# Performance work log

Measured on AMD Instinct MI355X. Metric: run time of the kernel, lower is better.

The kernel has to match this reference:

```python
import jax, jax.numpy as jnp
import numpy as np

B, T, HID = 1, 4096, 1024
H, HKV, D = 16, 4, 64          # query heads, kv heads, head_dim
G = H // HKV                    # gqa groups; repeat '(h g)' -> q head idx = h*G + g
EPS = 1e-6
SCALE = 1.0 / np.sqrt(D)


def setup_inputs() -> dict:
    key = jax.random.key(0)
    ks = jax.random.split(key, 8)
    hidden_states = jax.random.normal(ks[0], (B, T, HID), dtype=jnp.float32)
    # real rotary tables, shape [1, T, D//2]
    inv_freq = 1.0 / (10000.0 ** (jnp.arange(0, D // 2, dtype=jnp.float32) / (D // 2)))
    theta = jnp.arange(T, dtype=jnp.float32)[:, None] * inv_freq[None, :]
    cos = jnp.cos(theta)[None]
    sin = jnp.sin(theta)[None]
    s = 1.0 / np.sqrt(HID)
    Wq = jax.random.normal(ks[1], (HID, H * D), dtype=jnp.float32) * s
    Wk = jax.random.normal(ks[2], (HID, HKV * D), dtype=jnp.float32) * s
    Wv = jax.random.normal(ks[3], (HID, HKV * D), dtype=jnp.float32) * s
    Wo = jax.random.normal(ks[4], (H * D, HID), dtype=jnp.float32) * s
    q_norm_w = jnp.ones((D,), dtype=jnp.float32)
    k_norm_w = jnp.ones((D,), dtype=jnp.float32)
    return dict(hidden_states=hidden_states, cos=cos, sin=sin, Wq=Wq, Wk=Wk,
                Wv=Wv, Wo=Wo, q_norm_w=q_norm_w, k_norm_w=k_norm_w)


def _rmsnorm(x, w):
    xf = x.astype(jnp.float32)
    n = xf * jax.lax.rsqrt(jnp.mean(xf * xf, axis=-1, keepdims=True) + EPS)
    return (n * w).astype(x.dtype)


def _rope(x, cos, sin):
    # x: [b, t, h, d]; cos/sin: [1, t, d//2] -> [1, t, 1, d//2]
    half = x.shape[-1] // 2
    x1, x2 = x[..., :half], x[..., half:]
    c = cos[:, :x.shape[1], None, :]
    s = sin[:, :x.shape[1], None, :]
    return jnp.concatenate([x1 * c - x2 * s, x1 * s + x2 * c], axis=-1)


def reference(hidden_states, cos, sin, Wq, Wk, Wv, Wo, q_norm_w, k_norm_w):
    b, t, _ = hidden_states.shape
    q = (hidden_states @ Wq).reshape(b, t, H, D)
    k = (hidden_states @ Wk).reshape(b, t, HKV, D)
    v = (hidden_states @ Wv).reshape(b, t, HKV, D)
    q = _rmsnorm(q, q_norm_w)
    k = _rmsnorm(k, k_norm_w)
    q = _rope(q, cos, sin)
    k = _rope(k, cos, sin)
    # GQA without materializing repeated K/V: q head idx = kv_head*G + group
    qg = q.reshape(b, t, HKV, G, D)
    scores = jnp.einsum('bqhgd,bkhd->bhgqk', qg, k) * SCALE
    causal = jnp.tril(jnp.ones((t, t), dtype=bool))  # flex block_mask = causal decoder mask
    scores = jnp.where(causal, scores, jnp.finfo(scores.dtype).min)
    p = jax.nn.softmax(scores, axis=-1)
    out = jnp.einsum('bhgqk,bkhd->bqhgd', p, v).reshape(b, t, H * D)
    return out @ Wo
```

## Files before the change

### kernel.cpp

```cpp
#include <hip/hip_runtime.h>
#include <stdint.h>

#define TT 4096
#define HIDD 1024

typedef __attribute__((ext_vector_type(4))) float f32x4;
typedef __attribute__((ext_vector_type(8))) short s16x8;

static constexpr float kEps = 1e-6f;
static constexpr float kCsc = 0.125f * 1.44269504088896f;

static constexpr size_t OFF_HS   = 0;
static constexpr size_t OFF_WQKV = 8388608;
static constexpr size_t OFF_WO   = 11534336;
static constexpr size_t OFF_QKV  = 13631488;
static constexpr size_t OFF_Q    = 0;
static constexpr size_t OFF_K    = 8388608;
static constexpr size_t OFF_VT   = 38797312;
static constexpr size_t OFF_O    = 13631488;

__device__ __forceinline__ unsigned int pk_bf16(float a, float b) {
  union { float f; unsigned int u; } x, y;
  x.f = a; y.f = b;
  unsigned int lo = (x.u + 0x7fffu + ((x.u >> 16) & 1u)) >> 16;
  unsigned int hi = (y.u + 0x7fffu + ((y.u >> 16) & 1u)) >> 16;
  return (lo & 0xffffu) | (hi << 16);
}
__device__ __forceinline__ unsigned short bf16_1(float a) {
  union { float f; unsigned int u; } x; x.f = a;
  return (unsigned short)((x.u + 0x7fffu + ((x.u >> 16) & 1u)) >> 16);
}
__device__ __forceinline__ unsigned int cvtpk(float lo, float hi) {
  unsigned int r;
  asm("v_cvt_pk_bf16_f32 %0, %1, %2" : "=v"(r) : "v"(lo), "v"(hi));
  return r;
}
__device__ __forceinline__ void gload16(const void* g, void* l) {
  __builtin_amdgcn_global_load_lds(
      (const __attribute__((address_space(1))) unsigned int*)g,
      (__attribute__((address_space(3))) unsigned int*)l, 16, 0, 0);
}

__global__ void k_convert_hs(const float* __restrict__ hs, unsigned short* __restrict__ out) {
  int idx = blockIdx.x * 256 + threadIdx.x;
  int t = idx >> 7, kc = idx & 127;
  const float4* src = (const float4*)(hs + (size_t)t * HIDD + kc * 8);
  float4 a = src[0], b = src[1];
  int kcs = (kc & ~7) | ((kc & 7) ^ (t & 7));
  uint4 w;
  w.x = pk_bf16(a.x, a.y); w.y = pk_bf16(a.z, a.w);
  w.z = pk_bf16(b.x, b.y); w.w = pk_bf16(b.z, b.w);
  *(uint4*)(out + (size_t)t * HIDD + kcs * 8) = w;
}

__global__ void k_convert_w_all(const float* __restrict__ Wq, const float* __restrict__ Wk,
                                const float* __restrict__ Wv, const float* __restrict__ Wo,
                                unsigned short* __restrict__ wqkv, unsigned short* __restrict__ wo_t) {
  int b = blockIdx.x, tid = threadIdx.x;
  const float* W; unsigned short* outT; int nshift, idx;
  if (b < 512)      { W = Wq; outT = wqkv;                nshift = 10; idx = b * 256 + tid; }
  else if (b < 640) { W = Wk; outT = wqkv + 1024 * 1024;  nshift = 8;  idx = (b - 512) * 256 + tid; }
  else if (b < 768) { W = Wv; outT = wqkv + 1280 * 1024;  nshift = 8;  idx = (b - 640) * 256 + tid; }
  else              { W = Wo; outT = wo_t;                nshift = 10; idx = (b - 768) * 256 + tid; }
  int ncols = 1 << nshift;
  int kc = idx >> nshift, n = idx & (ncols - 1);
  float v[8];
#pragma unroll
  for (int e = 0; e < 8; ++e) v[e] = W[(size_t)(kc * 8 + e) * ncols + n];
  int kcs = (kc & ~7) | ((kc & 7) ^ (n & 7));
  uint4 w;
  w.x = pk_bf16(v[0], v[1]); w.y = pk_bf16(v[2], v[3]);
  w.z = pk_bf16(v[4], v[5]); w.w = pk_bf16(v[6], v[7]);
  *(uint4*)(outT + (size_t)n * HIDD + kcs * 8) = w;
}

__global__ __launch_bounds__(512) void k_gemm(const unsigned short* __restrict__ A,
                                              const unsigned short* __restrict__ Bt,
                                              float* __restrict__ C, int M, int N, int K) {
  __shared__ __attribute__((aligned(16))) unsigned short As[2][128 * 64];
  __shared__ __attribute__((aligned(16))) unsigned short Bs[2][128 * 64];
  const int tid = threadIdx.x;
  const int m0 = blockIdx.y * 128, n0 = blockIdx.x * 128;
  const int wid = tid >> 6, lane = tid & 63;
  const int g = lane >> 4, qi = lane & 15;
  const int wr = wid >> 2, wc = wid & 3;
  const int srow = tid >> 3, schk = tid & 7;
  f32x4 acc[4][2] = {};
  const int nkt = K >> 6;

  auto STAGE = [&](int b, int k0) {
#pragma unroll
    for (int j = 0; j < 2; ++j) {
      int ra = j * 64 + srow;
      gload16(A + (size_t)(m0 + ra) * K + k0 + schk * 8,
              (char*)&As[b][0] + j * 8192 + (wid << 10));
      gload16(Bt + (size_t)(n0 + ra) * K + k0 + schk * 8,
              (char*)&Bs[b][0] + j * 8192 + (wid << 10));
    }
  };

  STAGE(0, 0);
  __syncthreads();
  int cur = 0;
  for (int kt = 0; kt < nkt; ++kt) {
    if (kt + 1 < nkt) STAGE(cur ^ 1, (kt + 1) << 6);
#pragma unroll
    for (int kh = 0; kh < 2; ++kh) {
      s16x8 af[4], bq[2];
#pragma unroll
      for (int i = 0; i < 4; ++i) {
        int rA = wr * 64 + i * 16 + qi;
        af[i] = *(const s16x8*)((const char*)&As[cur][0] + rA * 128 + ((((kh << 2) | g) ^ (rA & 7)) << 4));
      }
#pragma unroll
      for (int jn = 0; jn < 2; ++jn) {
        int rB = wc * 32 + jn * 16 + qi;
        bq[jn] = *(const s16x8*)((const char*)&Bs[cur][0] + rB * 128 + ((((kh << 2) | g) ^ (rB & 7)) << 4));
      }
      __builtin_amdgcn_s_setprio(1);
#pragma unroll
      for (int i = 0; i < 4; ++i)
#pragma unroll
        for (int jn = 0; jn < 2; ++jn)
          acc[i][jn] = __builtin_amdgcn_mfma_f32_16x16x32_bf16(af[i], bq[jn], acc[i][jn], 0, 0, 0);
      __builtin_amdgcn_s_setprio(0);
    }
    __syncthreads();
    cur ^= 1;
  }
#pragma unroll
  for (int i = 0; i < 4; ++i)
#pragma unroll
    for (int jn = 0; jn < 2; ++jn) {
      int row = m0 + wr * 64 + i * 16 + g * 4;
      int col = n0 + wc * 32 + jn * 16 + qi;
#pragma unroll
      for (int r = 0; r < 4; ++r)
        C[(size_t)(row + r) * N + col] = acc[i][jn][r];
    }
}

__global__ void k_prep(const float* __restrict__ qkv, const float* __restrict__ cosb,
                       const float* __restrict__ sinb, const float* __restrict__ qw,
                       const float* __restrict__ kw, unsigned short* __restrict__ qo,
                       unsigned short* __restrict__ ko) {
  int rowid = blockIdx.x * 4 + (threadIdx.x >> 6);
  int lane = threadIdx.x & 63;
  int t = rowid / 20, slot = rowid % 20;
  float x = qkv[(size_t)t * 1536 + slot * 64 + lane];
  float ss = x * x;
#pragma unroll
  for (int off = 32; off; off >>= 1) ss += __shfl_xor(ss, off);
  float n = x * rsqrtf(ss * (1.0f / 64.0f) + kEps);
  n *= (slot < 16) ? qw[lane] : kw[lane];
  float c = cosb[t * 32 + (lane & 31)];
  float s = sinb[t * 32 + (lane & 31)];
  float other = __shfl_xor(n, 32);
  float r = (lane < 32) ? (n * c - other * s) : (other * s + n * c);
  if (slot < 16) {
    unsigned short b = bf16_1(r * kCsc);
    qo[((size_t)slot * TT + t) * 64 + lane] = b;
  } else {
    unsigned short b = bf16_1(r);
    int hv = slot - 16;
    int d = (((lane >> 3) ^ (t & 7)) << 3) | (lane & 7);
    ko[((size_t)hv * TT + t) * 64 + d] = b;
  }
}

__global__ void k_vT(const float* __restrict__ qkv, unsigned short* __restrict__ vt) {
  __shared__ float tile[64][65];
  int t0 = blockIdx.x * 64, hv = blockIdx.y, tid = threadIdx.x;
  int cc = tid & 63, rr0 = tid >> 6;
#pragma unroll
  for (int i = 0; i < 16; ++i) {
    int r = rr0 * 16 + i;
    tile[r][cc] = qkv[(size_t)(t0 + r) * 1536 + 1280 + hv * 64 + cc];
  }
  __syncthreads();
#pragma unroll
  for (int jj = 0; jj < 2; ++jj) {
    int idx = jj * 256 + tid;
    int d = idx >> 3, tc = idx & 7;
    uint4 w;
    w.x = pk_bf16(tile[tc * 8 + 0][d], tile[tc * 8 + 1][d]);
    w.y = pk_bf16(tile[tc * 8 + 2][d], tile[tc * 8 + 3][d]);
    w.z = pk_bf16(tile[tc * 8 + 4][d], tile[tc * 8 + 5][d]);
    w.w = pk_bf16(tile[tc * 8 + 6][d], tile[tc * 8 + 7][d]);
    int tcs = tc ^ (d & 7);
    *(uint4*)(vt + ((size_t)hv * 64 + d) * TT + t0 + tcs * 8) = w;
  }
}

__global__ __launch_bounds__(512) void k_attn(const unsigned short* __restrict__ q,
                                              const unsigned short* __restrict__ kk,
                                              const unsigned short* __restrict__ vt,
                                              unsigned short* __restrict__ o) {
  __shared__ __attribute__((aligned(16))) unsigned short Kl[2][64 * 64];
  __shared__ __attribute__((aligned(16))) unsigned short Vl[2][64 * 64];
  __shared__ __attribute__((aligned(16))) unsigned short Pl[8][1536];
  const int tid = threadIdx.x;
  const int bid = blockIdx.x;
  const int work = (bid & 7) * 64 + (bid >> 3);
  const int h = work >> 5;
  const int i0 = work & 31;
  const int hv = h >> 2;
  const int wid = tid >> 6, lane = tid & 63, g = lane >> 4, qi = lane & 15;
  const int qt = (wid < 4) ? i0 : (63 - i0);
  const int smax = 63 - i0;
  char* pb = (char*)&Pl[wid][0];

  auto STAGE = [&](int b, int s) {
    const int kv0 = s * 64;
    const int r = wid * 8 + (lane >> 3), c8 = (lane & 7) * 8;
    gload16(kk + ((size_t)hv * TT + kv0 + r) * 64 + c8, (char*)&Kl[b][0] + (wid << 10));
    gload16(vt + ((size_t)hv * 64 + r) * TT + kv0 + c8, (char*)&Vl[b][0] + (wid << 10));
  };

  const int qg = qt * 64 + (wid & 3) * 16 + qi;
  s16x8 qf[2];
#pragma unroll
  for (int kh = 0; kh < 2; ++kh)
    qf[kh] = *(const s16x8*)(q + ((size_t)h * TT + qg) * 64 + kh * 32 + g * 8);
  f32x4 acc[4] = {};
  float l0 = 0.0f, l1 = 0.0f;

  STAGE(0, 0);
  __syncthreads();
  int cur = 0;
  for (int s = 0; s <= smax; ++s) {
    if (s < smax) STAGE(cur ^ 1, s + 1);
    if (s <= qt) {
      const int kv0 = s * 64;
      f32x4 sacc[4] = {};
#pragma unroll
      for (int kh = 0; kh < 2; ++kh) {
        s16x8 kf[4];
#pragma unroll
        for (int cf = 0; cf < 4; ++cf) {
          int row = cf * 16 + qi;
          kf[cf] = *(const s16x8*)((const char*)&Kl[cur][0] + row * 128 + ((((kh << 2) | g) ^ (row & 7)) << 4));
        }
        __builtin_amdgcn_s_setprio(1);
#pragma unroll
        for (int cf = 0; cf < 4; ++cf)
          sacc[cf] = __builtin_amdgcn_mfma_f32_16x16x32_bf16(kf[cf], qf[kh], sacc[cf], 0, 0, 0);
        __builtin_amdgcn_s_setprio(0);
      }
      float pv[16];
      if (s == qt) {
#pragma unroll
        for (int cf = 0; cf < 4; ++cf)
#pragma unroll
          for (int r = 0; r < 4; ++r) {
            float v = sacc[cf][r];
            if ((kv0 + cf * 16 + g * 4 + r) > qg) v = -1e30f;
            pv[cf * 4 + r] = v;
          }
      } else {
#pragma unroll
        for (int cf = 0; cf < 4; ++cf)
#pragma unroll
          for (int r = 0; r < 4; ++r) pv[cf * 4 + r] = sacc[cf][r];
      }
#pragma unroll
      for (int i = 0; i < 8; ++i) {
        float e0 = exp2f(pv[2 * i]), e1 = exp2f(pv[2 * i + 1]);
        pv[2 * i] = e0; pv[2 * i + 1] = e1;
        l0 += e0; l1 += e1;
      }
#pragma unroll
      for (int cf = 0; cf < 4; ++cf) {
        int chunk = cf * 2 + (g >> 1);
        int base = qi * 128 + ((chunk ^ (qi & 7)) << 4) + ((g & 1) << 3);
        uint2 pw;
        pw.x = cvtpk(pv[cf * 4 + 0], pv[cf * 4 + 1]);
        pw.y = cvtpk(pv[cf * 4 + 2], pv[cf * 4 + 3]);
        *(uint2*)(pb + base) = pw;
      }
#pragma unroll
      for (int kh = 0; kh < 2; ++kh) {
        s16x8 pf = *(const s16x8*)(pb + qi * 128 + ((((kh << 2) | g) ^ (qi & 7)) << 4));
        s16x8 vf[4];
#pragma unroll
        for (int cf = 0; cf < 4; ++cf) {
          int row = cf * 16 + qi;
          vf[cf] = *(const s16x8*)((const char*)&Vl[cur][0] + row * 128 + ((((kh << 2) | g) ^ (row & 7)) << 4));
        }
        __builtin_amdgcn_s_setprio(1);
#pragma unroll
        for (int cf = 0; cf < 4; ++cf)
          acc[cf] = __builtin_amdgcn_mfma_f32_16x16x32_bf16(vf[cf], pf, acc[cf], 0, 0, 0);
        __builtin_amdgcn_s_setprio(0);
      }
    }
    __syncthreads();
    cur ^= 1;
  }
  float l_run = l0 + l1;
  l_run += __shfl_xor(l_run, 16);
  l_run += __shfl_xor(l_run, 32);
  float inv = 1.0f / l_run;
#pragma unroll
  for (int cf = 0; cf < 4; ++cf) {
    int col = h * 64 + cf * 16 + g * 4;
    int chunk = col >> 3;
    int chs = (chunk & ~7) | ((chunk & 7) ^ (qg & 7));
    char* ob = (char*)o + (size_t)qg * 2048 + (chs << 4) + ((g & 1) << 3);
    *(unsigned int*)ob = cvtpk(acc[cf][0] * inv, acc[cf][1] * inv);
    *(unsigned int*)(ob + 4) = cvtpk(acc[cf][2] * inv, acc[cf][3] * inv);
  }
}

extern "C" void kernel_launch(void* const* d_in, const int* in_sizes, int n_in,
                              void* d_out, int out_size, void* d_ws, size_t ws_size,
                              hipStream_t stream) {
  const float* hs   = (const float*)d_in[0];
  const float* cosb = (const float*)d_in[1];
  const float* sinb = (const float*)d_in[2];
  const float* Wq   = (const float*)d_in[3];
  const float* Wk   = (const float*)d_in[4];
  const float* Wv   = (const float*)d_in[5];
  const float* Wo   = (const float*)d_in[6];
  const float* qw   = (const float*)d_in[7];
  const float* kw   = (const float*)d_in[8];
  char* ws = (char*)d_ws;
  unsigned short* hs_swz = (unsigned short*)(ws + OFF_HS);
  unsigned short* wqkv   = (unsigned short*)(ws + OFF_WQKV);
  unsigned short* wo_t   = (unsigned short*)(ws + OFF_WO);
  float*          qkv    = (float*)(ws + OFF_QKV);
  unsigned short* qbf    = (unsigned short*)(ws + OFF_Q);
  unsigned short* kbf    = (unsigned short*)(ws + OFF_K);
  unsigned short* vtb    = (unsigned short*)(ws + OFF_VT);
  unsigned short* obf    = (unsigned short*)(ws + OFF_O);

  k_convert_hs<<<2048, 256, 0, stream>>>(hs, hs_swz);
  k_convert_w_all<<<1280, 256, 0, stream>>>(Wq, Wk, Wv, Wo, wqkv, wo_t);
  k_gemm<<<dim3(12, 32), 512, 0, stream>>>(hs_swz, wqkv, qkv, 4096, 1536, 1024);
  k_prep<<<20480, 256, 0, stream>>>(qkv, cosb, sinb, qw, kw, qbf, kbf);
  k_vT<<<dim3(64, 4), 256, 0, stream>>>(qkv, vtb);
  k_attn<<<512, 512, 0, stream>>>(qbf, kbf, vtb, obf);
  k_gemm<<<dim3(8, 32), 512, 0, stream>>>(obf, wo_t, (float*)d_out, 4096, 1024, 1024);
}
```

Baseline: 143.6 us.

## Restructure attention to per-wave 16-row tiles reading K/V directly from global

Attention no longer stages K and V tiles through double-buffered LDS with block-wide barriers. Each wave now owns 16-query-row tiles, taking one long and one short tile to balance the causal work, and reads K and V fragments directly from global or L2. V is stored in a tile-blocked transposed layout and K without the swizzle, so that these direct loads are contiguous. The loop is software-pipelined so that the softmax and P·V step of the previous block overlaps with the QK of the current one, and exp2 uses raw v_exp_f32. The goal is to remove the LDS staging and __syncthreads cost, at the price of more global traffic and register pressure, with launch bounds set for two blocks per CU.

```diff
diff --git a/kernel.cpp b/kernel.cpp
--- a/kernel.cpp
+++ b/kernel.cpp
@@ -33,6 +33,11 @@
 __device__ __forceinline__ unsigned int cvtpk(float lo, float hi) {
   unsigned int r;
   asm("v_cvt_pk_bf16_f32 %0, %1, %2" : "=v"(r) : "v"(lo), "v"(hi));
+  return r;
+}
+__device__ __forceinline__ float fexp2(float x) {
+  float r;
+  asm("v_exp_f32 %0, %1\n\ts_nop 0" : "=v"(r) : "v"(x));
   return r;
 }
 __device__ __forceinline__ void gload16(const void* g, void* l) {
@@ -163,14 +168,14 @@
   } else {
     unsigned short b = bf16_1(r);
     int hv = slot - 16;
-    int d = (((lane >> 3) ^ (t & 7)) << 3) | (lane & 7);
-    ko[((size_t)hv * TT + t) * 64 + d] = b;
+    ko[((size_t)hv * TT + t) * 64 + lane] = b;
   }
 }
 
 __global__ void k_vT(const float* __restrict__ qkv, unsigned short* __restrict__ vt) {
   __shared__ float tile[64][65];
   int t0 = blockIdx.x * 64, hv = blockIdx.y, tid = threadIdx.x;
+  int blk = blockIdx.x;
   int cc = tid & 63, rr0 = tid >> 6;
 #pragma unroll
   for (int i = 0; i < 16; ++i) {
@@ -187,86 +192,50 @@
     w.y = pk_bf16(tile[tc * 8 + 2][d], tile[tc * 8 + 3][d]);
     w.z = pk_bf16(tile[tc * 8 + 4][d], tile[tc * 8 + 5][d]);
     w.w = pk_bf16(tile[tc * 8 + 6][d], tile[tc * 8 + 7][d]);
-    int tcs = tc ^ (d & 7);
-    *(uint4*)(vt + ((size_t)hv * 64 + d) * TT + t0 + tcs * 8) = w;
-  }
-}
-
-__global__ __launch_bounds__(512) void k_attn(const unsigned short* __restrict__ q,
-                                              const unsigned short* __restrict__ kk,
-                                              const unsigned short* __restrict__ vt,
-                                              unsigned short* __restrict__ o) {
-  __shared__ __attribute__((aligned(16))) unsigned short Kl[2][64 * 64];
-  __shared__ __attribute__((aligned(16))) unsigned short Vl[2][64 * 64];
-  __shared__ __attribute__((aligned(16))) unsigned short Pl[8][1536];
+    *(uint4*)(vt + (((size_t)hv * 64 + blk) * 64 + d) * 64 + tc * 8) = w;
+  }
+}
+
+__global__ __launch_bounds__(512, 2) void k_attn(const unsigned short* __restrict__ q,
+                                                 const unsigned short* __restrict__ kk,
+                                                 const unsigned short* __restrict__ vt,
+                                                 unsigned short* __restrict__ o) {
+  __shared__ __attribute__((aligned(16))) unsigned short Pl[8][1024];
   const int tid = threadIdx.x;
+  const int wid = tid >> 6, lane = tid & 63, g = lane >> 4, qi = lane & 15;
   const int bid = blockIdx.x;
-  const int work = (bid & 7) * 64 + (bid >> 3);
-  const int h = work >> 5;
-  const int i0 = work & 31;
-  const int hv = h >> 2;
-  const int wid = tid >> 6, lane = tid & 63, g = lane >> 4, qi = lane & 15;
-  const int qt = (wid < 4) ? i0 : (63 - i0);
-  const int smax = 63 - i0;
+  const int xcd = bid & 7, blk = bid >> 3;
+  const int p = blk * 8 + wid;
+  const int head = xcd * 2 + (p >> 7);
+  const int aa = p & 127;
+  const int hv = head >> 2;
   char* pb = (char*)&Pl[wid][0];
-
-  auto STAGE = [&](int b, int s) {
-    const int kv0 = s * 64;
-    const int r = wid * 8 + (lane >> 3), c8 = (lane & 7) * 8;
-    gload16(kk + ((size_t)hv * TT + kv0 + r) * 64 + c8, (char*)&Kl[b][0] + (wid << 10));
-    gload16(vt + ((size_t)hv * 64 + r) * TT + kv0 + c8, (char*)&Vl[b][0] + (wid << 10));
-  };
-
-  const int qg = qt * 64 + (wid & 3) * 16 + qi;
-  s16x8 qf[2];
-#pragma unroll
-  for (int kh = 0; kh < 2; ++kh)
-    qf[kh] = *(const s16x8*)(q + ((size_t)h * TT + qg) * 64 + kh * 32 + g * 8);
-  f32x4 acc[4] = {};
-  float l0 = 0.0f, l1 = 0.0f;
-
-  STAGE(0, 0);
-  __syncthreads();
-  int cur = 0;
-  for (int s = 0; s <= smax; ++s) {
-    if (s < smax) STAGE(cur ^ 1, s + 1);
-    if (s <= qt) {
-      const int kv0 = s * 64;
-      f32x4 sacc[4] = {};
-#pragma unroll
-      for (int kh = 0; kh < 2; ++kh) {
-        s16x8 kf[4];
-#pragma unroll
-        for (int cf = 0; cf < 4; ++cf) {
-          int row = cf * 16 + qi;
-          kf[cf] = *(const s16x8*)((const char*)&Kl[cur][0] + row * 128 + ((((kh << 2) | g) ^ (row & 7)) << 4));
-        }
-        __builtin_amdgcn_s_setprio(1);
-#pragma unroll
-        for (int cf = 0; cf < 4; ++cf)
-          sacc[cf] = __builtin_amdgcn_mfma_f32_16x16x32_bf16(kf[cf], qf[kh], sacc[cf], 0, 0, 0);
-        __builtin_amdgcn_s_setprio(0);
-      }
-      float pv[16];
-      if (s == qt) {
-#pragma unroll
-        for (int cf = 0; cf < 4; ++cf)
-#pragma unroll
-          for (int r = 0; r < 4; ++r) {
-            float v = sacc[cf][r];
-            if ((kv0 + cf * 16 + g * 4 + r) > qg) v = -1e30f;
-            pv[cf * 4 + r] = v;
-          }
-      } else {
-#pragma unroll
-        for (int cf = 0; cf < 4; ++cf)
-#pragma unroll
-          for (int r = 0; r < 4; ++r) pv[cf * 4 + r] = sacc[cf][r];
-      }
-#pragma unroll
-      for (int i = 0; i < 8; ++i) {
-        float e0 = exp2f(pv[2 * i]), e1 = exp2f(pv[2 * i + 1]);
-        pv[2 * i] = e0; pv[2 * i + 1] = e1;
+  const unsigned short* kb = kk + ((size_t)hv * TT) * 64;
+
+  for (int half = 0; half < 2; ++half) {
+    const int t16 = half ? aa : (255 - aa);
+    const int nst = (t16 >> 2) + 1;
+    const int qg = t16 * 16 + qi;
+    s16x8 qf[2];
+#pragma unroll
+    for (int kh = 0; kh < 2; ++kh)
+      qf[kh] = *(const s16x8*)(q + ((size_t)head * TT + qg) * 64 + kh * 32 + g * 8);
+    f32x4 acc[4] = {};
+    float l0 = 0.0f, l1 = 0.0f;
+    float pv[16];
+
+    auto SMPV = [&](int s) {
+      const unsigned short* vb = vt + (((size_t)hv * 64 + s) * 64) * 64;
+      s16x8 vf[2][4];
+#pragma unroll
+      for (int kh = 0; kh < 2; ++kh)
+#pragma unroll
+        for (int cf = 0; cf < 4; ++cf)
+          vf[kh][cf] = *(const s16x8*)(vb + (size_t)(cf * 16 + qi) * 64 + kh * 32 + g * 8);
+#pragma unroll
+      for (int j = 0; j < 8; ++j) {
+        float e0 = fexp2(pv[2 * j]), e1 = fexp2(pv[2 * j + 1]);
+        pv[2 * j] = e0; pv[2 * j + 1] = e1;
         l0 += e0; l1 += e1;
       }
 #pragma unroll
@@ -281,34 +250,62 @@
 #pragma unroll
       for (int kh = 0; kh < 2; ++kh) {
         s16x8 pf = *(const s16x8*)(pb + qi * 128 + ((((kh << 2) | g) ^ (qi & 7)) << 4));
-        s16x8 vf[4];
-#pragma unroll
-        for (int cf = 0; cf < 4; ++cf) {
-          int row = cf * 16 + qi;
-          vf[cf] = *(const s16x8*)((const char*)&Vl[cur][0] + row * 128 + ((((kh << 2) | g) ^ (row & 7)) << 4));
-        }
         __builtin_amdgcn_s_setprio(1);
 #pragma unroll
         for (int cf = 0; cf < 4; ++cf)
-          acc[cf] = __builtin_amdgcn_mfma_f32_16x16x32_bf16(vf[cf], pf, acc[cf], 0, 0, 0);
+          acc[cf] = __builtin_amdgcn_mfma_f32_16x16x32_bf16(vf[kh][cf], pf, acc[cf], 0, 0, 0);
         __builtin_amdgcn_s_setprio(0);
       }
-    }
-    __syncthreads();
-    cur ^= 1;
-  }
-  float l_run = l0 + l1;
-  l_run += __shfl_xor(l_run, 16);
-  l_run += __shfl_xor(l_run, 32);
-  float inv = 1.0f / l_run;
-#pragma unroll
-  for (int cf = 0; cf < 4; ++cf) {
-    int col = h * 64 + cf * 16 + g * 4;
-    int chunk = col >> 3;
-    int chs = (chunk & ~7) | ((chunk & 7) ^ (qg & 7));
-    char* ob = (char*)o + (size_t)qg * 2048 + (chs << 4) + ((g & 1) << 3);
-    *(unsigned int*)ob = cvtpk(acc[cf][0] * inv, acc[cf][1] * inv);
-    *(unsigned int*)(ob + 4) = cvtpk(acc[cf][2] * inv, acc[cf][3] * inv);
+    };
+
+    for (int i = 0; i < nst; ++i) {
+      const int kv0 = i * 64;
+      s16x8 kf[2][4];
+#pragma unroll
+      for (int kh = 0; kh < 2; ++kh)
+#pragma unroll
+        for (int cf = 0; cf < 4; ++cf)
+          kf[kh][cf] = *(const s16x8*)(kb + (size_t)(kv0 + cf * 16 + qi) * 64 + kh * 32 + g * 8);
+      if (i > 0) SMPV(i - 1);
+      f32x4 sacc[4] = {};
+#pragma unroll
+      for (int kh = 0; kh < 2; ++kh) {
+        __builtin_amdgcn_s_setprio(1);
+#pragma unroll
+        for (int cf = 0; cf < 4; ++cf)
+          sacc[cf] = __builtin_amdgcn_mfma_f32_16x16x32_bf16(kf[kh][cf], qf[kh], sacc[cf], 0, 0, 0);
+        __builtin_amdgcn_s_setprio(0);
+      }
+      if (i == nst - 1) {
+#pragma unroll
+        for (int cf = 0; cf < 4; ++cf)
+#pragma unroll
+          for (int r = 0; r < 4; ++r) {
+            float v = sacc[cf][r];
+            pv[cf * 4 + r] = ((kv0 + cf * 16 + g * 4 + r) > qg) ? -1e30f : v;
+          }
+      } else {
+#pragma unroll
+        for (int cf = 0; cf < 4; ++cf)
+#pragma unroll
+          for (int r = 0; r < 4; ++r) pv[cf * 4 + r] = sacc[cf][r];
+      }
+    }
+    SMPV(nst - 1);
+
+    float l_run = l0 + l1;
+    l_run += __shfl_xor(l_run, 16);
+    l_run += __shfl_xor(l_run, 32);
+    float inv = 1.0f / l_run;
+#pragma unroll
+    for (int cf = 0; cf < 4; ++cf) {
+      int col = head * 64 + cf * 16 + g * 4;
+      int chunk = col >> 3;
+      int chs = (chunk & ~7) | ((chunk & 7) ^ (qg & 7));
+      char* ob = (char*)o + (size_t)qg * 2048 + (chs << 4) + ((g & 1) << 3);
+      *(unsigned int*)ob = cvtpk(acc[cf][0] * inv, acc[cf][1] * inv);
+      *(unsigned int*)(ob + 4) = cvtpk(acc[cf][2] * inv, acc[cf][3] * inv);
+    }
   }
 }
 
@@ -339,6 +336,6 @@
   k_gemm<<<dim3(12, 32), 512, 0, stream>>>(hs_swz, wqkv, qkv, 4096, 1536, 1024);
   k_prep<<<20480, 256, 0, stream>>>(qkv, cosb, sinb, qw, kw, qbf, kbf);
   k_vT<<<dim3(64, 4), 256, 0, stream>>>(qkv, vtb);
-  k_attn<<<512, 512, 0, stream>>>(qbf, kbf, vtb, obf);
+  k_attn<<<256, 512, 0, stream>>>(qbf, kbf, vtb, obf);
   k_gemm<<<dim3(8, 32), 512, 0, stream>>>(obf, wo_t, (float*)d_out, 4096, 1024, 1024);
 }
```

Result: slower. 302.5 us (+110.7%).

## Software-pipeline attention loop: overlap previous tile's softmax/PV with current QK

Applied to the files above, without the earlier changes.

Restructures the causal attention inner loop so the exp/softmax, P store and PV MFMAs for tile s-1 run after the K fragment loads for tile s and before its QK MFMAs. V fragments are preloaded into registers at the end of each step so they survive the double-buffer swap, and a trailing SMPV call drains the pipeline. The aim is to hide LDS load latency and exp work behind independent MFMA streams. In exchange it raises VGPR pressure (K and V fragments held together), which could reduce occupancy or cause spills.

```diff
diff --git a/kernel.cpp b/kernel.cpp
--- a/kernel.cpp
+++ b/kernel.cpp
@@ -224,79 +224,91 @@
     qf[kh] = *(const s16x8*)(q + ((size_t)h * TT + qg) * 64 + kh * 32 + g * 8);
   f32x4 acc[4] = {};
   float l0 = 0.0f, l1 = 0.0f;
+  float pv[16];
+  s16x8 vf[2][4];
+
+  auto SMPV = [&]() {
+#pragma unroll
+    for (int j = 0; j < 8; ++j) {
+      float e0 = exp2f(pv[2 * j]), e1 = exp2f(pv[2 * j + 1]);
+      pv[2 * j] = e0; pv[2 * j + 1] = e1;
+      l0 += e0; l1 += e1;
+    }
+#pragma unroll
+    for (int cf = 0; cf < 4; ++cf) {
+      int chunk = cf * 2 + (g >> 1);
+      int base = qi * 128 + ((chunk ^ (qi & 7)) << 4) + ((g & 1) << 3);
+      uint2 pw;
+      pw.x = cvtpk(pv[cf * 4 + 0], pv[cf * 4 + 1]);
+      pw.y = cvtpk(pv[cf * 4 + 2], pv[cf * 4 + 3]);
+      *(uint2*)(pb + base) = pw;
+    }
+#pragma unroll
+    for (int kh = 0; kh < 2; ++kh) {
+      s16x8 pf = *(const s16x8*)(pb + qi * 128 + ((((kh << 2) | g) ^ (qi & 7)) << 4));
+      __builtin_amdgcn_s_setprio(1);
+#pragma unroll
+      for (int cf = 0; cf < 4; ++cf)
+        acc[cf] = __builtin_amdgcn_mfma_f32_16x16x32_bf16(vf[kh][cf], pf, acc[cf], 0, 0, 0);
+      __builtin_amdgcn_s_setprio(0);
+    }
+  };
 
   STAGE(0, 0);
   __syncthreads();
   int cur = 0;
   for (int s = 0; s <= smax; ++s) {
     if (s < smax) STAGE(cur ^ 1, s + 1);
-    if (s <= qt) {
+    s16x8 kf[2][4];
+    const bool active = (s <= qt);
+    if (active) {
+#pragma unroll
+      for (int kh = 0; kh < 2; ++kh)
+#pragma unroll
+        for (int cf = 0; cf < 4; ++cf) {
+          int row = cf * 16 + qi;
+          kf[kh][cf] = *(const s16x8*)((const char*)&Kl[cur][0] + row * 128 + ((((kh << 2) | g) ^ (row & 7)) << 4));
+        }
+    }
+    if (s >= 1 && s <= qt + 1) SMPV();
+    if (active) {
       const int kv0 = s * 64;
       f32x4 sacc[4] = {};
 #pragma unroll
       for (int kh = 0; kh < 2; ++kh) {
-        s16x8 kf[4];
+        __builtin_amdgcn_s_setprio(1);
+#pragma unroll
+        for (int cf = 0; cf < 4; ++cf)
+          sacc[cf] = __builtin_amdgcn_mfma_f32_16x16x32_bf16(kf[kh][cf], qf[kh], sacc[cf], 0, 0, 0);
+        __builtin_amdgcn_s_setprio(0);
+      }
+      if (s == qt) {
+#pragma unroll
+        for (int cf = 0; cf < 4; ++cf)
+#pragma unroll
+          for (int r = 0; r < 4; ++r) {
+            float v = sacc[cf][r];
+            pv[cf * 4 + r] = ((kv0 + cf * 16 + g * 4 + r) > qg) ? -1e30f : v;
+          }
+      } else {
+#pragma unroll
+        for (int cf = 0; cf < 4; ++cf)
+#pragma unroll
+          for (int r = 0; r < 4; ++r) pv[cf * 4 + r] = sacc[cf][r];
+      }
+#pragma unroll
+      for (int kh = 0; kh < 2; ++kh)
 #pragma unroll
         for (int cf = 0; cf < 4; ++cf) {
           int row = cf * 16 + qi;
-          kf[cf] = *(const s16x8*)((const char*)&Kl[cur][0] + row * 128 + ((((kh << 2) | g) ^ (row & 7)) << 4));
+          vf[kh][cf] = *(const s16x8*)((const char*)&Vl[cur][0] + row * 128 + ((((kh << 2) | g) ^ (row & 7)) << 4));
         }
-        __builtin_amdgcn_s_setprio(1);
-#pragma unroll
-        for (int cf = 0; cf < 4; ++cf)
-          sacc[cf] = __builtin_amdgcn_mfma_f32_16x16x32_bf16(kf[cf], qf[kh], sacc[cf], 0, 0, 0);
-        __builtin_amdgcn_s_setprio(0);
-      }
-      float pv[16];
-      if (s == qt) {
-#pragma unroll
-        for (int cf = 0; cf < 4; ++cf)
-#pragma unroll
-          for (int r = 0; r < 4; ++r) {
-            float v = sacc[cf][r];
-            if ((kv0 + cf * 16 + g * 4 + r) > qg) v = -1e30f;
-            pv[cf * 4 + r] = v;
-          }
-      } else {
-#pragma unroll
-        for (int cf = 0; cf < 4; ++cf)
-#pragma unroll
-          for (int r = 0; r < 4; ++r) pv[cf * 4 + r] = sacc[cf][r];
-      }
-#pragma unroll
-      for (int i = 0; i < 8; ++i) {
-        float e0 = exp2f(pv[2 * i]), e1 = exp2f(pv[2 * i + 1]);
-        pv[2 * i] = e0; pv[2 * i + 1] = e1;
-        l0 += e0; l1 += e1;
-      }
-#pragma unroll
-      for (int cf = 0; cf < 4; ++cf) {
-        int chunk = cf * 2 + (g >> 1);
-        int base = qi * 128 + ((chunk ^ (qi & 7)) << 4) + ((g & 1) << 3);
-        uint2 pw;
-        pw.x = cvtpk(pv[cf * 4 + 0], pv[cf * 4 + 1]);
-        pw.y = cvtpk(pv[cf * 4 + 2], pv[cf * 4 + 3]);
-        *(uint2*)(pb + base) = pw;
-      }
-#pragma unroll
-      for (int kh = 0; kh < 2; ++kh) {
-        s16x8 pf = *(const s16x8*)(pb + qi * 128 + ((((kh << 2) | g) ^ (qi & 7)) << 4));
-        s16x8 vf[4];
-#pragma unroll
-        for (int cf = 0; cf < 4; ++cf) {
-          int row = cf * 16 + qi;
-          vf[cf] = *(const s16x8*)((const char*)&Vl[cur][0] + row * 128 + ((((kh << 2) | g) ^ (row & 7)) << 4));
-        }
-        __builtin_amdgcn_s_setprio(1);
-#pragma unroll
-        for (int cf = 0; cf < 4; ++cf)
-          acc[cf] = __builtin_amdgcn_mfma_f32_16x16x32_bf16(vf[cf], pf, acc[cf], 0, 0, 0);
-        __builtin_amdgcn_s_setprio(0);
-      }
     }
     __syncthreads();
     cur ^= 1;
   }
+  if (qt == smax) SMPV();
+
   float l_run = l0 + l1;
   l_run += __shfl_xor(l_run, 16);
   l_run += __shfl_xor(l_run, 32);
```

Measured after the change: 183.7 us. 1.28x slower.

## Split attention into smaller per-tile blocks and shrink GEMM tiles for occupancy

Applied to the files above, without the earlier changes.

The attention kernel changes from 512-thread blocks that paired complementary causal query tiles to 128-thread blocks. Each block handles one 64-row query tile, with every warp owning 32 query rows and reusing each K/V fragment across two MFMA row groups. Blocks are ordered longest-first and grouped by XCD to balance load. The GEMM moves to 256-thread blocks with 128x64 tiles, doubling the grid to raise occupancy and wave count, at the cost of less B-tile reuse per block.

```diff
diff --git a/kernel.cpp b/kernel.cpp
--- a/kernel.cpp
+++ b/kernel.cpp
@@ -74,28 +74,32 @@
   *(uint4*)(outT + (size_t)n * HIDD + kcs * 8) = w;
 }
 
-__global__ __launch_bounds__(512) void k_gemm(const unsigned short* __restrict__ A,
+__global__ __launch_bounds__(256) void k_gemm(const unsigned short* __restrict__ A,
                                               const unsigned short* __restrict__ Bt,
                                               float* __restrict__ C, int M, int N, int K) {
   __shared__ __attribute__((aligned(16))) unsigned short As[2][128 * 64];
-  __shared__ __attribute__((aligned(16))) unsigned short Bs[2][128 * 64];
+  __shared__ __attribute__((aligned(16))) unsigned short Bs[2][64 * 64];
   const int tid = threadIdx.x;
-  const int m0 = blockIdx.y * 128, n0 = blockIdx.x * 128;
+  const int m0 = blockIdx.y * 128, n0 = blockIdx.x * 64;
   const int wid = tid >> 6, lane = tid & 63;
   const int g = lane >> 4, qi = lane & 15;
-  const int wr = wid >> 2, wc = wid & 3;
-  const int srow = tid >> 3, schk = tid & 7;
+  const int wr = wid >> 1, wc = wid & 1;
+  const int srow = lane >> 3, schk = lane & 7;
   f32x4 acc[4][2] = {};
   const int nkt = K >> 6;
 
   auto STAGE = [&](int b, int k0) {
 #pragma unroll
+    for (int j = 0; j < 4; ++j) {
+      int ra = j * 32 + wid * 8 + srow;
+      gload16(A + (size_t)(m0 + ra) * K + k0 + schk * 8,
+              (char*)&As[b][0] + j * 4096 + (wid << 10));
+    }
+#pragma unroll
     for (int j = 0; j < 2; ++j) {
-      int ra = j * 64 + srow;
-      gload16(A + (size_t)(m0 + ra) * K + k0 + schk * 8,
-              (char*)&As[b][0] + j * 8192 + (wid << 10));
-      gload16(Bt + (size_t)(n0 + ra) * K + k0 + schk * 8,
-              (char*)&Bs[b][0] + j * 8192 + (wid << 10));
+      int rb = j * 32 + wid * 8 + srow;
+      gload16(Bt + (size_t)(n0 + rb) * K + k0 + schk * 8,
+              (char*)&Bs[b][0] + j * 4096 + (wid << 10));
     }
   };
 
@@ -192,123 +196,145 @@
   }
 }
 
-__global__ __launch_bounds__(512) void k_attn(const unsigned short* __restrict__ q,
-                                              const unsigned short* __restrict__ kk,
-                                              const unsigned short* __restrict__ vt,
-                                              unsigned short* __restrict__ o) {
+__global__ __launch_bounds__(128, 2) void k_attn(const unsigned short* __restrict__ q,
+                                                 const unsigned short* __restrict__ kk,
+                                                 const unsigned short* __restrict__ vt,
+                                                 unsigned short* __restrict__ o) {
   __shared__ __attribute__((aligned(16))) unsigned short Kl[2][64 * 64];
   __shared__ __attribute__((aligned(16))) unsigned short Vl[2][64 * 64];
-  __shared__ __attribute__((aligned(16))) unsigned short Pl[8][1536];
+  __shared__ __attribute__((aligned(16))) unsigned short Pl[2][2048];
   const int tid = threadIdx.x;
+  const int wid = tid >> 6, lane = tid & 63, g = lane >> 4, qi = lane & 15;
   const int bid = blockIdx.x;
-  const int work = (bid & 7) * 64 + (bid >> 3);
-  const int h = work >> 5;
-  const int i0 = work & 31;
-  const int hv = h >> 2;
-  const int wid = tid >> 6, lane = tid & 63, g = lane >> 4, qi = lane & 15;
-  const int qt = (wid < 4) ? i0 : (63 - i0);
-  const int smax = 63 - i0;
+  const int xcd = bid & 7, j = bid >> 3;
+  const int head = xcd * 2 + (j & 1);
+  const int qt = 63 - (j >> 1);
+  const int hv = head >> 2;
   char* pb = (char*)&Pl[wid][0];
+  const int srow = lane >> 3, schk8 = (lane & 7) * 8;
 
   auto STAGE = [&](int b, int s) {
     const int kv0 = s * 64;
-    const int r = wid * 8 + (lane >> 3), c8 = (lane & 7) * 8;
-    gload16(kk + ((size_t)hv * TT + kv0 + r) * 64 + c8, (char*)&Kl[b][0] + (wid << 10));
-    gload16(vt + ((size_t)hv * 64 + r) * TT + kv0 + c8, (char*)&Vl[b][0] + (wid << 10));
+#pragma unroll
+    for (int jj = 0; jj < 4; ++jj) {
+      int r = jj * 16 + wid * 8 + srow;
+      gload16(kk + ((size_t)hv * TT + kv0 + r) * 64 + schk8,
+              (char*)&Kl[b][0] + jj * 2048 + (wid << 10));
+      gload16(vt + ((size_t)hv * 64 + r) * TT + kv0 + schk8,
+              (char*)&Vl[b][0] + jj * 2048 + (wid << 10));
+    }
   };
 
-  const int qg = qt * 64 + (wid & 3) * 16 + qi;
-  s16x8 qf[2];
-#pragma unroll
-  for (int kh = 0; kh < 2; ++kh)
-    qf[kh] = *(const s16x8*)(q + ((size_t)h * TT + qg) * 64 + kh * 32 + g * 8);
-  f32x4 acc[4] = {};
-  float l0 = 0.0f, l1 = 0.0f;
+  const int qg0 = qt * 64 + wid * 32 + qi;
+  s16x8 qf[2][2];
+#pragma unroll
+  for (int t = 0; t < 2; ++t)
+#pragma unroll
+    for (int kh = 0; kh < 2; ++kh)
+      qf[t][kh] = *(const s16x8*)(q + ((size_t)head * TT + qg0 + t * 16) * 64 + kh * 32 + g * 8);
+  f32x4 acc[2][4] = {};
+  float lsum[2] = {0.0f, 0.0f};
 
   STAGE(0, 0);
   __syncthreads();
   int cur = 0;
-  for (int s = 0; s <= smax; ++s) {
-    if (s < smax) STAGE(cur ^ 1, s + 1);
-    if (s <= qt) {
-      const int kv0 = s * 64;
-      f32x4 sacc[4] = {};
-#pragma unroll
-      for (int kh = 0; kh < 2; ++kh) {
-        s16x8 kf[4];
-#pragma unroll
-        for (int cf = 0; cf < 4; ++cf) {
-          int row = cf * 16 + qi;
-          kf[cf] = *(const s16x8*)((const char*)&Kl[cur][0] + row * 128 + ((((kh << 2) | g) ^ (row & 7)) << 4));
-        }
-        __builtin_amdgcn_s_setprio(1);
+  for (int s = 0; s <= qt; ++s) {
+    if (s < qt) STAGE(cur ^ 1, s + 1);
+    const int kv0 = s * 64;
+    s16x8 kf[2][4];
+#pragma unroll
+    for (int kh = 0; kh < 2; ++kh)
+#pragma unroll
+      for (int cf = 0; cf < 4; ++cf) {
+        int row = cf * 16 + qi;
+        kf[kh][cf] = *(const s16x8*)((const char*)&Kl[cur][0] + row * 128 + ((((kh << 2) | g) ^ (qi & 7)) << 4));
+      }
+    f32x4 sacc[2][4] = {};
+#pragma unroll
+    for (int kh = 0; kh < 2; ++kh) {
+      __builtin_amdgcn_s_setprio(1);
+#pragma unroll
+      for (int cf = 0; cf < 4; ++cf) {
+        sacc[0][cf] = __builtin_amdgcn_mfma_f32_16x16x32_bf16(kf[kh][cf], qf[0][kh], sacc[0][cf], 0, 0, 0);
+        sacc[1][cf] = __builtin_amdgcn_mfma_f32_16x16x32_bf16(kf[kh][cf], qf[1][kh], sacc[1][cf], 0, 0, 0);
+      }
+      __builtin_amdgcn_s_setprio(0);
+    }
+    const bool diag = (s == qt);
+#pragma unroll
+    for (int t = 0; t < 2; ++t) {
+      float pv[16];
+      const int qg = qg0 + t * 16;
+      if (diag) {
 #pragma unroll
         for (int cf = 0; cf < 4; ++cf)
-          sacc[cf] = __builtin_amdgcn_mfma_f32_16x16x32_bf16(kf[cf], qf[kh], sacc[cf], 0, 0, 0);
-        __builtin_amdgcn_s_setprio(0);
-      }
-      float pv[16];
-      if (s == qt) {
-#pragma unroll
-        for (int cf = 0; cf < 4; ++cf)
 #pragma unroll
           for (int r = 0; r < 4; ++r) {
-            float v = sacc[cf][r];
-            if ((kv0 + cf * 16 + g * 4 + r) > qg) v = -1e30f;
-            pv[cf * 4 + r] = v;
+            float v = sacc[t][cf][r];
+            pv[cf * 4 + r] = ((kv0 + cf * 16 + g * 4 + r) > qg) ? -1e30f : v;
           }
       } else {
 #pragma unroll
         for (int cf = 0; cf < 4; ++cf)
 #pragma unroll
-          for (int r = 0; r < 4; ++r) pv[cf * 4 + r] = sacc[cf][r];
-      }
+          for (int r = 0; r < 4; ++r) pv[cf * 4 + r] = sacc[t][cf][r];
+      }
+      float l0 = 0.0f, l1 = 0.0f;
 #pragma unroll
       for (int i = 0; i < 8; ++i) {
         float e0 = exp2f(pv[2 * i]), e1 = exp2f(pv[2 * i + 1]);
         pv[2 * i] = e0; pv[2 * i + 1] = e1;
         l0 += e0; l1 += e1;
       }
+      lsum[t] += l0 + l1;
+      const int qrow = t * 16 + qi;
 #pragma unroll
       for (int cf = 0; cf < 4; ++cf) {
         int chunk = cf * 2 + (g >> 1);
-        int base = qi * 128 + ((chunk ^ (qi & 7)) << 4) + ((g & 1) << 3);
+        int base = qrow * 128 + ((chunk ^ (qi & 7)) << 4) + ((g & 1) << 3);
         uint2 pw;
         pw.x = cvtpk(pv[cf * 4 + 0], pv[cf * 4 + 1]);
         pw.y = cvtpk(pv[cf * 4 + 2], pv[cf * 4 + 3]);
         *(uint2*)(pb + base) = pw;
       }
-#pragma unroll
-      for (int kh = 0; kh < 2; ++kh) {
-        s16x8 pf = *(const s16x8*)(pb + qi * 128 + ((((kh << 2) | g) ^ (qi & 7)) << 4));
-        s16x8 vf[4];
-#pragma unroll
-        for (int cf = 0; cf < 4; ++cf) {
-          int row = cf * 16 + qi;
-          vf[cf] = *(const s16x8*)((const char*)&Vl[cur][0] + row * 128 + ((((kh << 2) | g) ^ (row & 7)) << 4));
-        }
-        __builtin_amdgcn_s_setprio(1);
-#pragma unroll
-        for (int cf = 0; cf < 4; ++cf)
-          acc[cf] = __builtin_amdgcn_mfma_f32_16x16x32_bf16(vf[cf], pf, acc[cf], 0, 0, 0);
-        __builtin_amdgcn_s_setprio(0);
-      }
+    }
+#pragma unroll
+    for (int kh = 0; kh < 2; ++kh) {
+      s16x8 vf[4];
+#pragma unroll
+      for (int cf = 0; cf < 4; ++cf) {
+        int row = cf * 16 + qi;
+        vf[cf] = *(const s16x8*)((const char*)&Vl[cur][0] + row * 128 + ((((kh << 2) | g) ^ (qi & 7)) << 4));
+      }
+      s16x8 pf0 = *(const s16x8*)(pb + (0 * 16 + qi) * 128 + ((((kh << 2) | g) ^ (qi & 7)) << 4));
+      s16x8 pf1 = *(const s16x8*)(pb + (1 * 16 + qi) * 128 + ((((kh << 2) | g) ^ (qi & 7)) << 4));
+      __builtin_amdgcn_s_setprio(1);
+#pragma unroll
+      for (int cf = 0; cf < 4; ++cf) {
+        acc[0][cf] = __builtin_amdgcn_mfma_f32_16x16x32_bf16(vf[cf], pf0, acc[0][cf], 0, 0, 0);
+        acc[1][cf] = __builtin_amdgcn_mfma_f32_16x16x32_bf16(vf[cf], pf1, acc[1][cf], 0, 0, 0);
+      }
+      __builtin_amdgcn_s_setprio(0);
     }
     __syncthreads();
     cur ^= 1;
   }
-  float l_run = l0 + l1;
-  l_run += __shfl_xor(l_run, 16);
-  l_run += __shfl_xor(l_run, 32);
-  float inv = 1.0f / l_run;
-#pragma unroll
-  for (int cf = 0; cf < 4; ++cf) {
-    int col = h * 64 + cf * 16 + g * 4;
-    int chunk = col >> 3;
-    int chs = (chunk & ~7) | ((chunk & 7) ^ (qg & 7));
-    char* ob = (char*)o + (size_t)qg * 2048 + (chs << 4) + ((g & 1) << 3);
-    *(unsigned int*)ob = cvtpk(acc[cf][0] * inv, acc[cf][1] * inv);
-    *(unsigned int*)(ob + 4) = cvtpk(acc[cf][2] * inv, acc[cf][3] * inv);
+#pragma unroll
+  for (int t = 0; t < 2; ++t) {
+    float l_run = lsum[t];
+    l_run += __shfl_xor(l_run, 16);
+    l_run += __shfl_xor(l_run, 32);
+    float inv = 1.0f / l_run;
+    const int qg = qg0 + t * 16;
+#pragma unroll
+    for (int cf = 0; cf < 4; ++cf) {
+      int col = head * 64 + cf * 16 + g * 4;
+      int chunk = col >> 3;
+      int chs = (chunk & ~7) | ((chunk & 7) ^ (qg & 7));
+      char* ob = (char*)o + (size_t)qg * 2048 + (chs << 4) + ((g & 1) << 3);
+      *(unsigned int*)ob = cvtpk(acc[t][cf][0] * inv, acc[t][cf][1] * inv);
+      *(unsigned int*)(ob + 4) = cvtpk(acc[t][cf][2] * inv, acc[t][cf][3] * inv);
+    }
   }
 }
 
@@ -336,9 +362,9 @@
 
   k_convert_hs<<<2048, 256, 0, stream>>>(hs, hs_swz);
   k_convert_w_all<<<1280, 256, 0, stream>>>(Wq, Wk, Wv, Wo, wqkv, wo_t);
-  k_gemm<<<dim3(12, 32), 512, 0, stream>>>(hs_swz, wqkv, qkv, 4096, 1536, 1024);
+  k_gemm<<<dim3(24, 32), 256, 0, stream>>>(hs_swz, wqkv, qkv, 4096, 1536, 1024);
   k_prep<<<20480, 256, 0, stream>>>(qkv, cosb, sinb, qw, kw, qbf, kbf);
   k_vT<<<dim3(64, 4), 256, 0, stream>>>(qkv, vtb);
-  k_attn<<<512, 512, 0, stream>>>(qbf, kbf, vtb, obf);
-  k_gemm<<<dim3(8, 32), 512, 0, stream>>>(obf, wo_t, (float*)d_out, 4096, 1024, 1024);
-}
+  k_attn<<<1024, 128, 0, stream>>>(qbf, kbf, vtb, obf);
+  k_gemm<<<dim3(16, 32), 256, 0, stream>>>(obf, wo_t, (float*)d_out, 4096, 1024, 1024);
+}
```

Result: slower. 169.0 us (+17.7%).
